# Kernel tuning notes

Measured on AMD Instinct MI355X. Metric: run time of the kernel, lower is better.

## Reference

```python
import jax, jax.numpy as jnp
import numpy as np

N_NODES = 1_000_000
N_EDGES = 16_000_000
N_FEAT = 128
NUM_GRAPHS = 8192


def setup_inputs() -> dict:
    key = jax.random.key(0)
    k_x, k_e, k_b, k_w, k_pw, k_pb = jax.random.split(key, 6)
    x = jax.random.normal(k_x, (N_NODES, N_FEAT), dtype=jnp.float32)
    edge_index = jax.random.randint(k_e, (2, N_EDGES), 0, N_NODES, dtype=jnp.int64)
    batch = jnp.sort(jax.random.randint(k_b, (N_NODES,), 0, NUM_GRAPHS, dtype=jnp.int64))
    # GCNConv lin weight (F -> 1, no bias), xavier-ish scale
    W = jax.random.normal(k_w, (N_FEAT, 1), dtype=jnp.float32) * (6.0 / (N_FEAT + 1)) ** 0.5
    # post_pool Linear(1, 1, bias=True)
    pp_w = jax.random.normal(k_pw, (1, 1), dtype=jnp.float32)
    pp_b = jax.random.normal(k_pb, (1,), dtype=jnp.float32) * 0.1
    return {"x": x, "W": W, "pp_w": pp_w, "pp_b": pp_b,
            "edge_index": edge_index, "batch": batch}


def reference(x, W, pp_w, pp_b, edge_index, batch):
    N = x.shape[0]
    h = x @ W  # [N, 1] — tiny feature after GCNConv projection
    # add self-loops (PyG GCNConv default)
    loops = jnp.arange(N, dtype=edge_index.dtype)
    src = jnp.concatenate([edge_index[0], loops])  # message sources (col j)
    dst = jnp.concatenate([edge_index[1], loops])  # aggregation targets (row i)
    # symmetric degree normalization: deg over targets incl. self-loops
    deg = jax.ops.segment_sum(jnp.ones(src.shape[0], dtype=h.dtype), dst,
                              num_segments=N)
    dinv = jnp.where(deg > 0, jax.lax.rsqrt(deg), 0.0)
    norm = dinv[src] * dinv[dst]  # [E+N]
    # gather -> normalize -> scatter-add
    agg = jax.ops.segment_sum(norm[:, None] * h[src], dst, num_segments=N)  # [N,1]
    # global_add_pool by graph id
    pooled = jax.ops.segment_sum(agg, batch, num_segments=NUM_GRAPHS)  # [G,1]
    return pooled @ pp_w.T + pp_b  # Linear(1,1)
```

## Files before the change

### kernel.cpp

```cpp
#include <hip/hip_runtime.h>
#include <hip/hip_fp16.h>

#define NUM_GRAPHS 8192
#define BSHIFT 12
#define BSIZE 4096
#define CHUNK 4096
#define NGRP 32
#define REPL 8
#define WINDOW 256
#define WPAD 257

__global__ void __launch_bounds__(256)
pair_scatter_kernel(const int* __restrict__ src, const int* __restrict__ dst,
                    int E, int nchunks, int NBUK, int capG,
                    unsigned* __restrict__ cursor, unsigned* __restrict__ slab) {
    __shared__ unsigned cnt[256];
    __shared__ unsigned lbase[256];
    __shared__ unsigned sbase[256];
    __shared__ unsigned staged[CHUNK];
    __shared__ unsigned char sbuck[CHUNK];
    __shared__ unsigned s_tot;

    const int4* s4 = (const int4*)src;
    const int4* d4 = (const int4*)dst;
    int E4 = E >> 2;
    int tid = threadIdx.x;
    int g = blockIdx.x & (NGRP - 1);

    for (int chunk = blockIdx.x; chunk < nchunks; chunk += gridDim.x) {
        cnt[tid] = 0; __syncthreads();
        int b4 = chunk * (CHUNK / 4);
        int4 vd[4], vs[4];
        unsigned short r[16];
        #pragma unroll
        for (int k = 0; k < 4; ++k) {
            int idx = b4 + k * 256 + tid;
            if (idx < E4) { vd[k] = d4[idx]; vs[k] = s4[idx]; }
            else          { vd[k] = make_int4(-1, -1, -1, -1); }
        }
        #pragma unroll
        for (int k = 0; k < 4; ++k) {
            if (vd[k].x >= 0) {
                r[4*k+0] = (unsigned short)atomicAdd(&cnt[vd[k].x >> BSHIFT], 1u);
                r[4*k+1] = (unsigned short)atomicAdd(&cnt[vd[k].y >> BSHIFT], 1u);
                r[4*k+2] = (unsigned short)atomicAdd(&cnt[vd[k].z >> BSHIFT], 1u);
                r[4*k+3] = (unsigned short)atomicAdd(&cnt[vd[k].w >> BSHIFT], 1u);
            }
        }
        __syncthreads();
        lbase[tid] = cnt[tid]; __syncthreads();
        #pragma unroll
        for (int off = 1; off < 256; off <<= 1) {
            unsigned a = (tid >= off) ? lbase[tid - off] : 0u;
            __syncthreads();
            lbase[tid] += a;
            __syncthreads();
        }
        if (tid == 255) s_tot = lbase[255];
        if (tid < NBUK && cnt[tid])
            sbase[tid] = atomicAdd(&cursor[g * 256 + tid], cnt[tid]);
        unsigned excl = lbase[tid] - cnt[tid];
        __syncthreads();
        lbase[tid] = excl;
        __syncthreads();

        #pragma unroll
        for (int k = 0; k < 4; ++k) {
            if (vd[k].x >= 0) {
                int d0 = vd[k].x, d1 = vd[k].y, d2 = vd[k].z, d3 = vd[k].w;
                unsigned b0 = (unsigned)d0 >> BSHIFT, b1 = (unsigned)d1 >> BSHIFT;
                unsigned b2 = (unsigned)d2 >> BSHIFT, b3 = (unsigned)d3 >> BSHIFT;
                unsigned p0 = lbase[b0] + r[4*k+0];
                unsigned p1 = lbase[b1] + r[4*k+1];
                unsigned p2 = lbase[b2] + r[4*k+2];
                unsigned p3 = lbase[b3] + r[4*k+3];
                staged[p0] = ((unsigned)(d0 & (BSIZE-1)) << 20) | (unsigned)vs[k].x;
                staged[p1] = ((unsigned)(d1 & (BSIZE-1)) << 20) | (unsigned)vs[k].y;
                staged[p2] = ((unsigned)(d2 & (BSIZE-1)) << 20) | (unsigned)vs[k].z;
                staged[p3] = ((unsigned)(d3 & (BSIZE-1)) << 20) | (unsigned)vs[k].w;
                sbuck[p0] = (unsigned char)b0;
                sbuck[p1] = (unsigned char)b1;
                sbuck[p2] = (unsigned char)b2;
                sbuck[p3] = (unsigned char)b3;
            }
        }
        __syncthreads();
        unsigned tot = s_tot;
        for (unsigned pos = tid; pos < tot; pos += 256) {
            unsigned b = sbuck[pos];
            unsigned gp = sbase[b] + (pos - lbase[b]);
            if (gp < (unsigned)capG)
                slab[((size_t)g * NBUK + b) * capG + gp] = staged[pos];
        }
        __syncthreads();
    }
    if (blockIdx.x == 0 && tid < (E & 3)) {
        int i = (E & ~3) + tid;
        int d = dst[i];
        unsigned b = (unsigned)d >> BSHIFT;
        unsigned p = atomicAdd(&cursor[b], 1u);
        if (p < (unsigned)capG)
            slab[(size_t)b * capG + p] =
                ((unsigned)(d & (BSIZE-1)) << 20) | (unsigned)src[i];
    }
}

__global__ void __launch_bounds__(512)
hist_kernel(const unsigned* __restrict__ slab, int capG,
            const unsigned* __restrict__ cursor,
            unsigned* __restrict__ deg0, unsigned* __restrict__ deg1,
            int N, int NBUK) {
    __shared__ unsigned hist[BSIZE];
    int bp = blockIdx.x, tid = threadIdx.x;
    int b = bp >> 1, half = bp & 1;
    for (int t = tid; t < BSIZE; t += 512) hist[t] = 0;
    __syncthreads();

    int g0 = half * 16;
    for (int gg = g0; gg < g0 + 16; gg += 8) {
        unsigned n[8], maxn = 0;
        const unsigned* sp[8];
        #pragma unroll
        for (int k = 0; k < 8; ++k) {
            unsigned nn = cursor[(gg + k) * 256 + b];
            if (nn > (unsigned)capG) nn = capG;
            n[k] = nn; if (nn > maxn) maxn = nn;
            sp[k] = slab + ((size_t)(gg + k) * NBUK + b) * capG;
        }
        for (unsigned i = tid; i < maxn; i += 512) {
            unsigned e[8];
            #pragma unroll
            for (int k = 0; k < 8; ++k) e[k] = (i < n[k]) ? sp[k][i] : 0xFFFFFFFFu;
            #pragma unroll
            for (int k = 0; k < 8; ++k)
                if (e[k] != 0xFFFFFFFFu) atomicAdd(&hist[e[k] >> 20], 1u);
        }
    }
    __syncthreads();
    int base = b << BSHIFT;
    int lim = N - base; if (lim > BSIZE) lim = BSIZE;
    unsigned* degP = half ? deg1 : deg0;
    for (int t = tid; t < lim; t += 512) degP[base + t] = hist[t];
}

__global__ void node_kernel(const float* __restrict__ x,
                            const float* __restrict__ W,
                            const unsigned* __restrict__ deg0,
                            const unsigned* __restrict__ deg1,
                            const int* __restrict__ batch,
                            unsigned short* __restrict__ hsh,
                            unsigned* __restrict__ pkw, int N) {
    int gwave = (blockIdx.x * blockDim.x + threadIdx.x) >> 6;
    int lane = threadIdx.x & 63;
    int half = lane >> 5;
    int l32  = lane & 31;
    int total_waves = (gridDim.x * blockDim.x) >> 6;
    float4 wv = ((const float4*)W)[l32];
    for (int node = gwave * 2 + half; node < N; node += total_waves * 2) {
        float4 xv = ((const float4*)(x + (size_t)node * 128))[l32];
        float v = xv.x * wv.x + xv.y * wv.y + xv.z * wv.z + xv.w * wv.w;
        #pragma unroll
        for (int d = 16; d >= 1; d >>= 1) v += __shfl_xor(v, d);
        if (l32 == 0) {
            float di = rsqrtf((float)(deg0[node] + deg1[node] + 1u));
            hsh[node] = __half_as_ushort(__float2half(di * v));
            pkw[node] = ((unsigned)batch[node] << 16) |
                        __half_as_ushort(__float2half(di));
        }
    }
}

__global__ void __launch_bounds__(512)
aggregate_kernel(const unsigned* __restrict__ slab, int capG,
                 const unsigned* __restrict__ cursor,
                 const unsigned* __restrict__ pkw,
                 const unsigned short* __restrict__ hsh,
                 float* __restrict__ pooled, int N, int NBUK) {
    __shared__ unsigned pkw_s[BSIZE];
    __shared__ float win[REPL * WPAD];
    int bp = blockIdx.x, tid = threadIdx.x;
    int b = bp >> 2, q = bp & 3;
    int base = b << BSHIFT;
    int lim = N - base; if (lim > BSIZE) lim = BSIZE;

    for (int t = tid; t < BSIZE; t += 512) pkw_s[t] = (t < lim) ? pkw[base + t] : 0u;
    for (int t = tid; t < REPL * WPAD; t += 512) win[t] = 0.0f;
    __syncthreads();
    int g_lo = (int)(pkw_s[0] >> 16);
    int g_hi = (lim > 0) ? (int)(pkw_s[lim - 1] >> 16) : g_lo;
    int width = g_hi - g_lo + 1;
    bool windowed = (width <= WINDOW);
    int r = tid & (REPL - 1);

    int n0 = q * (BSIZE / 4);
    int n1 = (q + 1) * (BSIZE / 4); if (n1 > lim) n1 = lim;
    for (int t = n0 + tid; t < n1; t += 512) {
        unsigned w = pkw_s[t];
        float di = __half2float(__ushort_as_half((unsigned short)(w & 0xFFFFu)));
        float c = di * __half2float(__ushort_as_half(hsh[base + t]));
        if (windowed) atomicAdd(&win[r * WPAD + ((w >> 16) - g_lo)], c);
        else          atomicAdd(&pooled[w >> 16], c);
    }

    int g0 = q * 8;
    unsigned n[8], maxn = 0;
    const unsigned* sp[8];
    #pragma unroll
    for (int k = 0; k < 8; ++k) {
        unsigned nn = cursor[(g0 + k) * 256 + b];
        if (nn > (unsigned)capG) nn = capG;
        n[k] = nn; if (nn > maxn) maxn = nn;
        sp[k] = slab + ((size_t)(g0 + k) * NBUK + b) * capG;
    }
    for (unsigned i = tid; i < maxn; i += 512) {
        unsigned e[8]; bool v[8];
        #pragma unroll
        for (int k = 0; k < 8; ++k) { v[k] = (i < n[k]); e[k] = v[k] ? sp[k][i] : 0u; }
        unsigned w[8];
        #pragma unroll
        for (int k = 0; k < 8; ++k) w[k] = pkw_s[e[k] >> 20];
        unsigned short hb[8];
        #pragma unroll
        for (int k = 0; k < 8; ++k) hb[k] = hsh[e[k] & 0xFFFFFu];
        #pragma unroll
        for (int k = 0; k < 8; ++k) {
            float hv = __half2float(__ushort_as_half(hb[k]));
            float di = __half2float(__ushort_as_half((unsigned short)(w[k] & 0xFFFFu)));
            float c = v[k] ? hv * di : 0.0f;
            if (windowed) atomicAdd(&win[r * WPAD + ((w[k] >> 16) - g_lo)], c);
            else if (v[k]) atomicAdd(&pooled[w[k] >> 16], c);
        }
    }
    __syncthreads();
    if (windowed) {
        for (int g = tid; g < width; g += 512) {
            float s = 0.0f;
            #pragma unroll
            for (int rr = 0; rr < REPL; ++rr) s += win[rr * WPAD + g];
            atomicAdd(&pooled[g_lo + g], s);
        }
    }
}

__global__ void out_kernel(const float* __restrict__ pooled,
                           const float* __restrict__ pp_w,
                           const float* __restrict__ pp_b,
                           float* __restrict__ out) {
    int g = blockIdx.x * blockDim.x + threadIdx.x;
    if (g < NUM_GRAPHS) out[g] = pooled[g] * pp_w[0] + pp_b[0];
}

__global__ void deg_atomic_kernel(const int* __restrict__ dst, int E,
                                  unsigned* __restrict__ deg) {
    int tid = blockIdx.x * blockDim.x + threadIdx.x;
    int stride = gridDim.x * blockDim.x;
    for (int i = tid; i < E; i += stride) atomicAdd(&deg[dst[i]], 1u);
}

__global__ void node_fb_kernel(const float* __restrict__ x,
                               const float* __restrict__ W,
                               const unsigned* __restrict__ deg,
                               const int* __restrict__ batch,
                               unsigned short* __restrict__ hsh,
                               unsigned* __restrict__ pkw, int N) {
    int gtid = blockIdx.x * blockDim.x + threadIdx.x;
    int wave = gtid >> 6;
    int lane = threadIdx.x & 63;
    int half = lane >> 5;
    int l32  = lane & 31;
    int node = wave * 2 + half;
    if (node >= N) return;
    float4 xv = ((const float4*)(x + (size_t)node * 128))[l32];
    float4 wv = ((const float4*)W)[l32];
    float v = xv.x * wv.x + xv.y * wv.y + xv.z * wv.z + xv.w * wv.w;
    #pragma unroll
    for (int d = 16; d >= 1; d >>= 1) v += __shfl_xor(v, d);
    if (l32 == 0) {
        float di = rsqrtf((float)(deg[node] + 1u));
        hsh[node] = __half_as_ushort(__float2half(di * v));
        pkw[node] = ((unsigned)batch[node] << 16) | __half_as_ushort(__float2half(di));
    }
}

__global__ void pool_self_fb_kernel(const unsigned short* __restrict__ hsh,
                                    const unsigned* __restrict__ pkw,
                                    float* __restrict__ pooled, int N) {
    int i = blockIdx.x * blockDim.x + threadIdx.x;
    if (i >= N) return;
    unsigned w = pkw[i];
    float di = __half2float(__ushort_as_half((unsigned short)(w & 0xFFFFu)));
    atomicAdd(&pooled[w >> 16], di * __half2float(__ushort_as_half(hsh[i])));
}

__global__ void __launch_bounds__(512)
edge_direct_kernel(const int* __restrict__ src, const int* __restrict__ dst, int E,
                   const unsigned short* __restrict__ hsh,
                   const unsigned* __restrict__ pkw,
                   float* __restrict__ pooled) {
    __shared__ float pool[NUM_GRAPHS];
    for (int g = threadIdx.x; g < NUM_GRAPHS; g += 512) pool[g] = 0.0f;
    __syncthreads();
    int tid = blockIdx.x * 512 + threadIdx.x;
    int stride = gridDim.x * 512;
    for (int i = tid; i < E; i += stride) {
        unsigned w = pkw[dst[i]];
        float c = __half2float(__ushort_as_half(hsh[src[i]])) *
                  __half2float(__ushort_as_half((unsigned short)(w & 0xFFFFu)));
        atomicAdd(&pool[w >> 16], c);
    }
    __syncthreads();
    for (int g = threadIdx.x; g < NUM_GRAPHS; g += 512)
        if (pool[g] != 0.0f) atomicAdd(&pooled[g], pool[g]);
}

extern "C" void kernel_launch(void* const* d_in, const int* in_sizes, int n_in,
                              void* d_out, int out_size, void* d_ws, size_t ws_size,
                              hipStream_t stream) {
    const float* x    = (const float*)d_in[0];
    const float* W    = (const float*)d_in[1];
    const float* pp_w = (const float*)d_in[2];
    const float* pp_b = (const float*)d_in[3];
    const int*   ei   = (const int*)d_in[4];
    const int*   batch= (const int*)d_in[5];
    float* out = (float*)d_out;

    const int E = in_sizes[4] / 2;
    const int N = in_sizes[5];
    const int* src = ei;
    const int* dst = ei + E;
    int NBUK = (N + BSIZE - 1) >> BSHIFT;
    int nchunks = (E + CHUNK - 1) / CHUNK;

    char* ws = (char*)d_ws;
    size_t off = 0;
    auto alloc = [&](size_t bytes) {
        size_t o = off; off = (off + bytes + 255) & ~(size_t)255; return o;
    };
    size_t zero_bytes = (size_t)NUM_GRAPHS * 4 + (size_t)NGRP * 256 * 4;
    size_t zero_off   = alloc(zero_bytes);
    float*    pooled = (float*)(ws + zero_off);
    unsigned* cursor = (unsigned*)(ws + zero_off + (size_t)NUM_GRAPHS * 4);

    size_t deg0_off = alloc((size_t)N * 4);
    size_t deg1_off = alloc((size_t)N * 4);
    size_t hsh_off  = alloc((size_t)N * 2);
    size_t pkw_off  = alloc((size_t)N * 4);

    int meanG = E / (NBUK * NGRP) + 1;
    int capG = (meanG + meanG / 8 + 512 + 3) & ~3;
    size_t slab_off = alloc((size_t)NGRP * NBUK * (size_t)capG * 4);

    bool fast_ok = (NBUK <= 256) && (N <= (1 << 20)) && (off <= ws_size);

    unsigned*       deg0 = (unsigned*)(ws + deg0_off);
    unsigned*       deg1 = (unsigned*)(ws + deg1_off);
    unsigned short* hsh  = (unsigned short*)(ws + hsh_off);
    unsigned*       pkw  = (unsigned*)(ws + pkw_off);
    unsigned*       slab = (unsigned*)(ws + slab_off);

    hipMemsetAsync(ws + zero_off, 0, zero_bytes, stream);

    if (fast_ok) {
        int grid = nchunks < 4096 ? nchunks : 4096;
        pair_scatter_kernel<<<grid, 256, 0, stream>>>(src, dst, E, nchunks, NBUK,
                                                      capG, cursor, slab);
        hist_kernel<<<2 * NBUK, 512, 0, stream>>>(slab, capG, cursor,
                                                  deg0, deg1, N, NBUK);
        node_kernel<<<8192, 256, 0, stream>>>(x, W, deg0, deg1, batch, hsh, pkw, N);
        aggregate_kernel<<<4 * NBUK, 512, 0, stream>>>(slab, capG, cursor, pkw,
                                                       hsh, pooled, N, NBUK);
    } else {
        hipMemsetAsync(deg0, 0, (size_t)N * 4, stream);
        deg_atomic_kernel<<<2048, 256, 0, stream>>>(dst, E, deg0);
        int node_blocks = (N + 7) / 8;
        node_fb_kernel<<<node_blocks, 256, 0, stream>>>(x, W, deg0, batch, hsh, pkw, N);
        pool_self_fb_kernel<<<(N + 255) / 256, 256, 0, stream>>>(hsh, pkw, pooled, N);
        edge_direct_kernel<<<512, 512, 0, stream>>>(src, dst, E, hsh, pkw, pooled);
    }

    out_kernel<<<(NUM_GRAPHS + 255) / 256, 256, 0, stream>>>(pooled, pp_w, pp_b, out);
}
```

Baseline: 292.5 us.

## Overlap degree histogram with node projection; use wave-shuffle prefix scan

The degree histogram and the x@W projection now run in one launch, with separate block ranges doing each job. Because the projection no longer waits on the histogram, its roughly 512 MB read of x can proceed while the histogram blocks run. The raw projection is stored as float, and a small finalize kernel then applies rsqrt(deg) and packs the half-precision outputs, which adds one extra pass over N. In the scatter kernel, the 256-entry block-wide Hillis-Steele scan with many __syncthreads is replaced by a single-wave shuffle scan.

After: 276.2 us. 1.06x faster.

```diff
diff --git a/kernel.cpp b/kernel.cpp
--- a/kernel.cpp
+++ b/kernel.cpp
@@ -9,6 +9,7 @@
 #define REPL 8
 #define WINDOW 256
 #define WPAD 257
+#define FNT 512
 
 __global__ void __launch_bounds__(256)
 pair_scatter_kernel(const int* __restrict__ src, const int* __restrict__ dst,
@@ -48,20 +49,23 @@
             }
         }
         __syncthreads();
-        lbase[tid] = cnt[tid]; __syncthreads();
-        #pragma unroll
-        for (int off = 1; off < 256; off <<= 1) {
-            unsigned a = (tid >= off) ? lbase[tid - off] : 0u;
-            __syncthreads();
-            lbase[tid] += a;
-            __syncthreads();
-        }
-        if (tid == 255) s_tot = lbase[255];
+        if (tid < 64) {
+            unsigned run = 0;
+            for (int c0 = 0; c0 < 256; c0 += 64) {
+                unsigned v = cnt[c0 + tid];
+                unsigned s = v;
+                #pragma unroll
+                for (int off = 1; off < 64; off <<= 1) {
+                    unsigned o = __shfl_up(s, off);
+                    if (tid >= off) s += o;
+                }
+                lbase[c0 + tid] = run + s - v;
+                run += __shfl(s, 63);
+            }
+            if (tid == 0) s_tot = run;
+        }
         if (tid < NBUK && cnt[tid])
             sbase[tid] = atomicAdd(&cursor[g * 256 + tid], cnt[tid]);
-        unsigned excl = lbase[tid] - cnt[tid];
-        __syncthreads();
-        lbase[tid] = excl;
         __syncthreads();
 
         #pragma unroll
@@ -105,68 +109,74 @@
     }
 }
 
-__global__ void __launch_bounds__(512)
-hist_kernel(const unsigned* __restrict__ slab, int capG,
-            const unsigned* __restrict__ cursor,
-            unsigned* __restrict__ deg0, unsigned* __restrict__ deg1,
-            int N, int NBUK) {
+__global__ void __launch_bounds__(FNT)
+hist_h_kernel(const unsigned* __restrict__ slab, int capG,
+              const unsigned* __restrict__ cursor,
+              unsigned* __restrict__ deg0, unsigned* __restrict__ deg1,
+              const float* __restrict__ x, const float* __restrict__ W,
+              float* __restrict__ h, int N, int NBUK, int nhblocks) {
     __shared__ unsigned hist[BSIZE];
     int bp = blockIdx.x, tid = threadIdx.x;
-    int b = bp >> 1, half = bp & 1;
-    for (int t = tid; t < BSIZE; t += 512) hist[t] = 0;
-    __syncthreads();
-
-    int g0 = half * 16;
-    for (int gg = g0; gg < g0 + 16; gg += 8) {
-        unsigned n[8], maxn = 0;
-        const unsigned* sp[8];
-        #pragma unroll
-        for (int k = 0; k < 8; ++k) {
-            unsigned nn = cursor[(gg + k) * 256 + b];
-            if (nn > (unsigned)capG) nn = capG;
-            n[k] = nn; if (nn > maxn) maxn = nn;
-            sp[k] = slab + ((size_t)(gg + k) * NBUK + b) * capG;
-        }
-        for (unsigned i = tid; i < maxn; i += 512) {
-            unsigned e[8];
+
+    if (bp < 2 * NBUK) {
+        int b = bp >> 1, half = bp & 1;
+        for (int t = tid; t < BSIZE; t += FNT) hist[t] = 0;
+        __syncthreads();
+        int g0 = half * 16;
+        for (int gg = g0; gg < g0 + 16; gg += 8) {
+            unsigned n[8], maxn = 0;
+            const unsigned* sp[8];
             #pragma unroll
-            for (int k = 0; k < 8; ++k) e[k] = (i < n[k]) ? sp[k][i] : 0xFFFFFFFFu;
+            for (int k = 0; k < 8; ++k) {
+                unsigned nn = cursor[(gg + k) * 256 + b];
+                if (nn > (unsigned)capG) nn = capG;
+                n[k] = nn; if (nn > maxn) maxn = nn;
+                sp[k] = slab + ((size_t)(gg + k) * NBUK + b) * capG;
+            }
+            for (unsigned i = tid; i < maxn; i += FNT) {
+                unsigned e[8];
+                #pragma unroll
+                for (int k = 0; k < 8; ++k) e[k] = (i < n[k]) ? sp[k][i] : 0xFFFFFFFFu;
+                #pragma unroll
+                for (int k = 0; k < 8; ++k)
+                    if (e[k] != 0xFFFFFFFFu) atomicAdd(&hist[e[k] >> 20], 1u);
+            }
+        }
+        __syncthreads();
+        int base = b << BSHIFT;
+        int lim = N - base; if (lim > BSIZE) lim = BSIZE;
+        unsigned* degP = half ? deg1 : deg0;
+        for (int t = tid; t < lim; t += FNT) degP[base + t] = hist[t];
+    } else {
+        int hb = bp - 2 * NBUK;
+        int gwave = (hb * FNT + tid) >> 6;
+        int lane = tid & 63;
+        int half = lane >> 5;
+        int l32  = lane & 31;
+        int total_waves = (nhblocks * FNT) >> 6;
+        float4 wv = ((const float4*)W)[l32];
+        for (int node = gwave * 2 + half; node < N; node += total_waves * 2) {
+            float4 xv = ((const float4*)(x + (size_t)node * 128))[l32];
+            float v = xv.x * wv.x + xv.y * wv.y + xv.z * wv.z + xv.w * wv.w;
             #pragma unroll
-            for (int k = 0; k < 8; ++k)
-                if (e[k] != 0xFFFFFFFFu) atomicAdd(&hist[e[k] >> 20], 1u);
-        }
-    }
-    __syncthreads();
-    int base = b << BSHIFT;
-    int lim = N - base; if (lim > BSIZE) lim = BSIZE;
-    unsigned* degP = half ? deg1 : deg0;
-    for (int t = tid; t < lim; t += 512) degP[base + t] = hist[t];
-}
-
-__global__ void node_kernel(const float* __restrict__ x,
-                            const float* __restrict__ W,
-                            const unsigned* __restrict__ deg0,
-                            const unsigned* __restrict__ deg1,
-                            const int* __restrict__ batch,
-                            unsigned short* __restrict__ hsh,
-                            unsigned* __restrict__ pkw, int N) {
-    int gwave = (blockIdx.x * blockDim.x + threadIdx.x) >> 6;
-    int lane = threadIdx.x & 63;
-    int half = lane >> 5;
-    int l32  = lane & 31;
-    int total_waves = (gridDim.x * blockDim.x) >> 6;
-    float4 wv = ((const float4*)W)[l32];
-    for (int node = gwave * 2 + half; node < N; node += total_waves * 2) {
-        float4 xv = ((const float4*)(x + (size_t)node * 128))[l32];
-        float v = xv.x * wv.x + xv.y * wv.y + xv.z * wv.z + xv.w * wv.w;
-        #pragma unroll
-        for (int d = 16; d >= 1; d >>= 1) v += __shfl_xor(v, d);
-        if (l32 == 0) {
-            float di = rsqrtf((float)(deg0[node] + deg1[node] + 1u));
-            hsh[node] = __half_as_ushort(__float2half(di * v));
-            pkw[node] = ((unsigned)batch[node] << 16) |
-                        __half_as_ushort(__float2half(di));
-        }
+            for (int d = 16; d >= 1; d >>= 1) v += __shfl_xor(v, d);
+            if (l32 == 0) h[node] = v;
+        }
+    }
+}
+
+__global__ void finalize_kernel(const float* __restrict__ h,
+                                const unsigned* __restrict__ deg0,
+                                const unsigned* __restrict__ deg1,
+                                const int* __restrict__ batch,
+                                unsigned short* __restrict__ hsh,
+                                unsigned* __restrict__ pkw, int N) {
+    int i = blockIdx.x * blockDim.x + threadIdx.x;
+    int stride = gridDim.x * blockDim.x;
+    for (; i < N; i += stride) {
+        float di = rsqrtf((float)(deg0[i] + deg1[i] + 1u));
+        hsh[i] = __half_as_ushort(__float2half(di * h[i]));
+        pkw[i] = ((unsigned)batch[i] << 16) | __half_as_ushort(__float2half(di));
     }
 }
 
@@ -341,6 +351,7 @@
     float*    pooled = (float*)(ws + zero_off);
     unsigned* cursor = (unsigned*)(ws + zero_off + (size_t)NUM_GRAPHS * 4);
 
+    size_t h_off    = alloc((size_t)N * 4);
     size_t deg0_off = alloc((size_t)N * 4);
     size_t deg1_off = alloc((size_t)N * 4);
     size_t hsh_off  = alloc((size_t)N * 2);
@@ -352,6 +363,7 @@
 
     bool fast_ok = (NBUK <= 256) && (N <= (1 << 20)) && (off <= ws_size);
 
+    float*          h    = (float*)(ws + h_off);
     unsigned*       deg0 = (unsigned*)(ws + deg0_off);
     unsigned*       deg1 = (unsigned*)(ws + deg1_off);
     unsigned short* hsh  = (unsigned short*)(ws + hsh_off);
@@ -364,9 +376,10 @@
         int grid = nchunks < 4096 ? nchunks : 4096;
         pair_scatter_kernel<<<grid, 256, 0, stream>>>(src, dst, E, nchunks, NBUK,
                                                       capG, cursor, slab);
-        hist_kernel<<<2 * NBUK, 512, 0, stream>>>(slab, capG, cursor,
-                                                  deg0, deg1, N, NBUK);
-        node_kernel<<<8192, 256, 0, stream>>>(x, W, deg0, deg1, batch, hsh, pkw, N);
+        int nhblocks = 2048;
+        hist_h_kernel<<<2 * NBUK + nhblocks, FNT, 0, stream>>>(
+            slab, capG, cursor, deg0, deg1, x, W, h, N, NBUK, nhblocks);
+        finalize_kernel<<<1024, 256, 0, stream>>>(h, deg0, deg1, batch, hsh, pkw, N);
         aggregate_kernel<<<4 * NBUK, 512, 0, stream>>>(slab, capG, cursor, pkw,
                                                        hsh, pooled, N, NBUK);
     } else {
```
